# Kernel tuning notes

Measured on AMD Instinct MI355X. Metric: run time of the kernel, lower is better.

## Reference

```python
import jax, jax.numpy as jnp
import numpy as np

B = 512      # number of groups (samples)
SEG = 128    # points per group (fixed for the reference)
N = B * SEG  # total points
E = 64       # embed_size
D = 5 * E    # point feature dim = 320
L = 3        # pointNet blocks
MF = 2       # multiple_factor -> hidden = D*MF = 640
NEG_SLOPE = 0.01


def _leaky(x):
    return jnp.where(x >= 0, x, NEG_SLOPE * x)


def _mlp(x, W1, b1, W2, b2):
    # Linear -> LeakyReLU -> (Dropout=identity, eval) -> Linear -> LeakyReLU
    return _leaky(_leaky(x @ W1 + b1) @ W2 + b2)


def setup_inputs() -> dict:
    key = jax.random.key(0)
    ks = jax.random.split(key, 16)
    s = 0.02
    words = jax.random.randint(ks[0], (N, 5), 0, 26, dtype=jnp.int32)
    lengths = jnp.full((B,), SEG, dtype=jnp.int32)
    seg2all = jnp.repeat(jnp.arange(B, dtype=jnp.int32), SEG)
    inp = {
        "words": words,
        "lengths": lengths,
        "seg2all": seg2all,
        "embed": s * jax.random.normal(ks[1], (26, E), jnp.float32),
        "pu_W1": s * jax.random.normal(ks[2], (L, D, D * MF), jnp.float32),
        "pu_b1": jnp.zeros((L, D * MF), jnp.float32),
        "pu_W2": s * jax.random.normal(ks[3], (L, D * MF, D), jnp.float32),
        "pu_b2": jnp.zeros((L, D), jnp.float32),
        "gu_W1": s * jax.random.normal(ks[4], (L, D, D * MF), jnp.float32),
        "gu_b1": jnp.zeros((L, D * MF), jnp.float32),
        "gu_W2": s * jax.random.normal(ks[5], (L, D * MF, D), jnp.float32),
        "gu_b2": jnp.zeros((L, D), jnp.float32),
        "c_W": s * jax.random.normal(ks[6], (L, 2 * D, D), jnp.float32),
        "c_b": jnp.zeros((L, D), jnp.float32),
        "o_W1": s * jax.random.normal(ks[7], (D, D * MF), jnp.float32),
        "o_b1": jnp.zeros((D * MF,), jnp.float32),
        "o_W2": s * jax.random.normal(ks[8], (D * MF, 1), jnp.float32),
        "o_b2": jnp.zeros((1,), jnp.float32),
        "w": jnp.float32(0.13663686),
    }
    return inp


def reference(words, lengths, seg2all, embed, pu_W1, pu_b1, pu_W2, pu_b2,
              gu_W1, gu_b1, gu_W2, gu_b2, c_W, c_b, o_W1, o_b1, o_W2, o_b2, w):
    inv_len = 1.0 / lengths.astype(jnp.float32)  # [B]

    def seg_mean(x):  # segment_csr(x, offsets, reduce='mean')
        sums = jax.ops.segment_sum(x, seg2all, num_segments=B)
        return sums * inv_len[:, None]

    out = embed[words].reshape(-1, D)  # [N, D]
    for i in range(L):
        h = _mlp(out, pu_W1[i], pu_b1[i], pu_W2[i], pu_b2[i])          # point update
        g = _mlp(seg_mean(h), gu_W1[i], gu_b1[i], gu_W2[i], gu_b2[i])  # group update
        cat = jnp.concatenate([h, g[seg2all]], axis=1)                 # gather-back concat
        out = _leaky(cat @ c_W[i] + c_b[i]) + out                      # combine + residual
    y = _mlp(seg_mean(out), o_W1, o_b1, o_W2, o_b2)  # [B, 1]
    return y.squeeze(-1) + w * jnp.log2(lengths.astype(jnp.float32))
```

## Files before the change

### kernel.cpp

```cpp
#include <hip/hip_runtime.h>
#include <hip/hip_bf16.h>

using bf16 = __hip_bfloat16;
typedef short bf16x8 __attribute__((ext_vector_type(8)));
typedef float f32x4  __attribute__((ext_vector_type(4)));
typedef unsigned short u16;

__device__ __forceinline__ float leakyf(float x) { return x >= 0.f ? x : 0.01f * x; }

__device__ __forceinline__ float b2f(u16 u) {
  union { unsigned int i; float f; } c; c.i = (unsigned int)u << 16; return c.f;
}
__device__ __forceinline__ u16 f2b(float f) {
  __hip_bfloat16 h = __float2bfloat16(f);
  return *reinterpret_cast<u16*>(&h);
}

typedef const __attribute__((address_space(1))) unsigned int* gp_t;
typedef __attribute__((address_space(3))) unsigned int* lp_t;
__device__ __forceinline__ void gload16(const void* g, void* l) {
  __builtin_amdgcn_global_load_lds((gp_t)g, (lp_t)l, 16, 0, 0);
}

__global__ void pack_tiles(const float* __restrict__ pu1, const float* __restrict__ pu2,
                           const float* __restrict__ cw,
                           bf16* __restrict__ W0, bf16* __restrict__ W1t,
                           bf16* __restrict__ W4) {
  int job = blockIdx.y, type = job / 3, l = job % 3;
  int f = blockIdx.x * 256 + threadIdx.x;
  const float* s; bf16* d; int ld, nchunks;
  if (type == 0)      { nchunks = 25600; s = pu1 + (size_t)l * 204800; d = W0  + (size_t)l * 204800; ld = 640; }
  else if (type == 1) { nchunks = 25600; s = pu2 + (size_t)l * 204800; d = W1t + (size_t)l * 204800; ld = 320; }
  else                { nchunks = 12800; s = cw  + (size_t)l * 204800; d = W4  + (size_t)l * 102400; ld = 320; }
  if (f >= nchunks) return;
  int i  = f & 15;
  int ch = (f >> 4) & 7;
  int nt = (f >> 7) % 20;
  int sl = (f >> 7) / 20;
  int k, col;
  if (type == 0) { k = (sl % 5) * 64 + ch * 8; col = (sl / 5) * 320 + nt * 16 + i; }
  else           { k = sl * 64 + ch * 8;       col = nt * 16 + i; }
  bf16 v[8];
#pragma unroll
  for (int j = 0; j < 8; ++j)
    v[j] = __float2bfloat16(s[(size_t)(k + j) * ld + col]);
  *(bf16x8*)(d + (size_t)f * 8) = *(bf16x8*)v;
}

__global__ void pack_nmaj(const float* __restrict__ gu1, const float* __restrict__ gu2,
                          const float* __restrict__ cw, const float* __restrict__ ow1,
                          bf16* __restrict__ Wg1, bf16* __restrict__ Wg2,
                          bf16* __restrict__ Wg3, bf16* __restrict__ Wo1) {
  int job = blockIdx.y;
  int f = blockIdx.x * 256 + threadIdx.x;
  const float* s; bf16* d; int K, ld, nchunks, koff = 0;
  if (job < 3)       { int l = job;     K = 320; ld = 640; nchunks = 25600; s = gu1 + (size_t)l * 204800; d = Wg1 + (size_t)l * 204800; }
  else if (job < 6)  { int l = job - 3; K = 640; ld = 320; nchunks = 25600; s = gu2 + (size_t)l * 204800; d = Wg2 + (size_t)l * 204800; }
  else if (job < 9)  { int l = job - 6; K = 320; ld = 320; nchunks = 12800; s = cw  + (size_t)l * 204800; d = Wg3 + (size_t)l * 102400; koff = 320; }
  else               {                  K = 320; ld = 640; nchunks = 25600; s = ow1;                      d = Wo1; }
  if (f >= nchunks) return;
  int kc8 = K >> 3;
  int n = f / kc8, kc = f % kc8;
  bf16 v[8];
#pragma unroll
  for (int j = 0; j < 8; ++j)
    v[j] = __float2bfloat16(s[(size_t)(koff + kc * 8 + j) * ld + n]);
  *(bf16x8*)(d + (size_t)f * 8) = *(bf16x8*)v;
}

#define PWROW(vv, comp) { int row = rb + vv; \
  *(short*)((char*)p + row * 128 + (col2 ^ ((row & 7) << 4))) = (short)(fq.comp); }

__device__ __forceinline__ void paneWrite4(short* p, ushort4 f0, ushort4 f1,
                                           ushort4 f2, ushort4 f3,
                                           int r, int wc, int i16, int kg) {
  const int col2 = (wc * 16 + i16) * 2;
  { ushort4 fq = f0; int rb = r * 64 + 0  + kg * 4; PWROW(0, x) PWROW(1, y) PWROW(2, z) PWROW(3, w) }
  { ushort4 fq = f1; int rb = r * 64 + 16 + kg * 4; PWROW(0, x) PWROW(1, y) PWROW(2, z) PWROW(3, w) }
  { ushort4 fq = f2; int rb = r * 64 + 32 + kg * 4; PWROW(0, x) PWROW(1, y) PWROW(2, z) PWROW(3, w) }
  { ushort4 fq = f3; int rb = r * 64 + 48 + kg * 4; PWROW(0, x) PWROW(1, y) PWROW(2, z) PWROW(3, w) }
}

__device__ __forceinline__ void stageW(const bf16* src, short* dst, int wave, int lane) {
#pragma unroll
  for (int t = 0; t < 5; ++t) {
    int ci = (t * 8 + wave) * 64 + lane;
    gload16(src + (size_t)ci * 8, (char*)dst + (t * 8 + wave) * 1024);
  }
}

__device__ __forceinline__ void sliceMFMA(f32x4 (&acc)[4][5], const short* pn,
                                          const short* wb,
                                          int r, int wc, int i16, int kg) {
#pragma unroll
  for (int kk = 0; kk < 2; ++kk) {
    bf16x8 a[4];
#pragma unroll
    for (int m = 0; m < 4; ++m) {
      int row = r * 64 + m * 16 + i16;
      a[m] = *(const bf16x8*)((const char*)pn + row * 128 +
                              (((kk * 32 + kg * 8) * 2) ^ ((row & 7) << 4)));
    }
#pragma unroll
    for (int t = 0; t < 5; ++t) {
      bf16x8 b = *(const bf16x8*)((const char*)wb +
                                  (((wc + 4 * t) * 8 + kk * 4 + kg) << 8) + (i16 << 4));
#pragma unroll
      for (int m = 0; m < 4; ++m)
        acc[m][t] = __builtin_amdgcn_mfma_f32_16x16x32_bf16(a[m], b, acc[m][t], 0, 0, 0);
    }
  }
}

__device__ __forceinline__ float dotWrow(const bf16* __restrict__ w,
                                         const float* __restrict__ x, int K8) {
  float s = 0.f;
#pragma unroll 4
  for (int kb = 0; kb < K8; ++kb) {
    bf16x8 wv = *(const bf16x8*)(w + kb * 8);
#pragma unroll
    for (int u = 0; u < 8; ++u)
      s += b2f((u16)wv[u]) * x[kb * 8 + u];
  }
  return s;
}

__device__ __forceinline__ ushort4 pack4(float a, float b, float c, float d) {
  ushort4 u; u.x = f2b(a); u.y = f2b(b); u.z = f2b(c); u.w = f2b(d); return u;
}

__global__ __launch_bounds__(512, 2)
void fused_k(const int* __restrict__ words, const int* __restrict__ lengths,
             const float* __restrict__ embed,
             const bf16* __restrict__ W0, const bf16* __restrict__ W1t,
             const bf16* __restrict__ W4,
             const bf16* __restrict__ Wg1, const bf16* __restrict__ Wg2,
             const bf16* __restrict__ Wg3, const bf16* __restrict__ Wo1,
             const float* __restrict__ pb1, const float* __restrict__ pb2,
             const float* __restrict__ gb1, const float* __restrict__ gb2,
             const float* __restrict__ cb,  const float* __restrict__ ob1,
             const float* __restrict__ oW2, const float* __restrict__ ob2,
             const float* __restrict__ wsc, float* __restrict__ yout)
{
  __shared__ short pane[2][8192];
  __shared__ short wbuf[2][20480];
  __shared__ float embL[1664];
  __shared__ int   wrdL[640];
  __shared__ float mvec[320];
  __shared__ float tvec[640];
  __shared__ float gvec[320];
  __shared__ float redA[320];
  __shared__ float redB[320];
  __shared__ float redH[8];

  const int g    = blockIdx.x;
  const int tid  = threadIdx.x;
  const int wave = tid >> 6, lane = tid & 63;
  const int r    = wave >> 2, wc = wave & 3;
  const int i16  = lane & 15, kg = lane >> 4;
  const float invLen = 1.0f / (float)lengths[g];

  for (int i = tid; i < 1664; i += 512) embL[i] = embed[i];
  { const int* ws = words + (size_t)g * 640;
    for (int i = tid; i < 640; i += 512) wrdL[i] = ws[i]; }
  __syncthreads();

  ushort4 outf[4][5];
#pragma unroll
  for (int m = 0; m < 4; ++m) {
    int row = r * 64 + m * 16 + kg * 4;
#pragma unroll
    for (int t = 0; t < 5; ++t) {
      int col = (wc + 4 * t) * 16 + i16;
      int w = col >> 6, e = col & 63;
      outf[m][t] = pack4(embL[wrdL[(row + 0) * 5 + w] * 64 + e],
                         embL[wrdL[(row + 1) * 5 + w] * 64 + e],
                         embL[wrdL[(row + 2) * 5 + w] * 64 + e],
                         embL[wrdL[(row + 3) * 5 + w] * 64 + e]);
    }
  }

  for (int l = 0; l < 3; ++l) {
    ushort4 h1f[2][4][5];
#pragma unroll
    for (int p = 0; p < 2; ++p) {
      f32x4 acc[4][5];
#pragma unroll
      for (int m = 0; m < 4; ++m)
#pragma unroll
        for (int t = 0; t < 5; ++t) acc[m][t] = {0.f, 0.f, 0.f, 0.f};
      const bf16* wsrc = W0 + ((size_t)(l * 2 + p) * 5) * 20480;
      __syncthreads();
      stageW(wsrc, wbuf[0], wave, lane);
      paneWrite4(pane[0], outf[0][0], outf[1][0], outf[2][0], outf[3][0], r, wc, i16, kg);
#pragma unroll
      for (int ks = 0; ks < 5; ++ks) {
        __syncthreads();
        if (ks < 4) {
          stageW(wsrc + (size_t)(ks + 1) * 20480, wbuf[(ks + 1) & 1], wave, lane);
          paneWrite4(pane[(ks + 1) & 1], outf[0][ks + 1], outf[1][ks + 1],
                     outf[2][ks + 1], outf[3][ks + 1], r, wc, i16, kg);
        }
        sliceMFMA(acc, pane[ks & 1], wbuf[ks & 1], r, wc, i16, kg);
      }
#pragma unroll
      for (int t = 0; t < 5; ++t) {
        int col = p * 320 + (wc + 4 * t) * 16 + i16;
        float bv = pb1[l * 640 + col];
#pragma unroll
        for (int m = 0; m < 4; ++m)
          h1f[p][m][t] = pack4(leakyf(acc[m][t][0] + bv), leakyf(acc[m][t][1] + bv),
                               leakyf(acc[m][t][2] + bv), leakyf(acc[m][t][3] + bv));
      }
    }

    ushort4 hf[4][5];
    {
      f32x4 acc[4][5];
#pragma unroll
      for (int m = 0; m < 4; ++m)
#pragma unroll
        for (int t = 0; t < 5; ++t) acc[m][t] = {0.f, 0.f, 0.f, 0.f};
      const bf16* wsrc = W1t + (size_t)l * 10 * 20480;
      __syncthreads();
      stageW(wsrc, wbuf[0], wave, lane);
      paneWrite4(pane[0], h1f[0][0][0], h1f[0][1][0], h1f[0][2][0], h1f[0][3][0], r, wc, i16, kg);
#pragma unroll
      for (int ks = 0; ks < 10; ++ks) {
        __syncthreads();
        if (ks < 9) {
          stageW(wsrc + (size_t)(ks + 1) * 20480, wbuf[(ks + 1) & 1], wave, lane);
          const int p2 = (ks + 1) / 5, t2 = (ks + 1) % 5;
          paneWrite4(pane[(ks + 1) & 1], h1f[p2][0][t2], h1f[p2][1][t2],
                     h1f[p2][2][t2], h1f[p2][3][t2], r, wc, i16, kg);
        }
        sliceMFMA(acc, pane[ks & 1], wbuf[ks & 1], r, wc, i16, kg);
      }
      __syncthreads();
      float csum[5];
#pragma unroll
      for (int t = 0; t < 5; ++t) {
        int col = (wc + 4 * t) * 16 + i16;
        float bv = pb2[l * 320 + col];
        float v0 = leakyf(acc[0][t][0] + bv), v1 = leakyf(acc[0][t][1] + bv);
        float v2 = leakyf(acc[0][t][2] + bv), v3 = leakyf(acc[0][t][3] + bv);
        float cs = v0 + v1 + v2 + v3;
        hf[0][t] = pack4(v0, v1, v2, v3);
#pragma unroll
        for (int m = 1; m < 4; ++m) {
          float w0 = leakyf(acc[m][t][0] + bv), w1 = leakyf(acc[m][t][1] + bv);
          float w2 = leakyf(acc[m][t][2] + bv), w3 = leakyf(acc[m][t][3] + bv);
          cs += w0 + w1 + w2 + w3;
          hf[m][t] = pack4(w0, w1, w2, w3);
        }
        csum[t] = cs;
      }
#pragma unroll
      for (int t = 0; t < 5; ++t) {
        float s = csum[t];
        s += __shfl_xor(s, 16);
        s += __shfl_xor(s, 32);
        if (kg == 0) (r ? redB : redA)[(wc + 4 * t) * 16 + i16] = s;
      }
      __syncthreads();
      if (tid < 320) mvec[tid] = (redA[tid] + redB[tid]) * invLen;
      __syncthreads();
    }

    tvec[tid] = leakyf(dotWrow(Wg1 + ((size_t)l * 640 + tid) * 320, mvec, 40) +
                       gb1[l * 640 + tid]);
    if (tid < 128) {
      int j2 = 512 + tid;
      tvec[j2] = leakyf(dotWrow(Wg1 + ((size_t)l * 640 + j2) * 320, mvec, 40) +
                        gb1[l * 640 + j2]);
    }
    __syncthreads();
    if (tid < 320)
      gvec[tid] = leakyf(dotWrow(Wg2 + ((size_t)l * 320 + tid) * 640, tvec, 80) +
                         gb2[l * 320 + tid]);
    __syncthreads();
    if (tid < 320)
      tvec[tid] = dotWrow(Wg3 + ((size_t)l * 320 + tid) * 320, gvec, 40) +
                  cb[l * 320 + tid];
    __syncthreads();

    {
      f32x4 acc[4][5];
#pragma unroll
      for (int m = 0; m < 4; ++m)
#pragma unroll
        for (int t = 0; t < 5; ++t) acc[m][t] = {0.f, 0.f, 0.f, 0.f};
      const bf16* wsrc = W4 + (size_t)l * 5 * 20480;
      __syncthreads();
      stageW(wsrc, wbuf[0], wave, lane);
      paneWrite4(pane[0], hf[0][0], hf[1][0], hf[2][0], hf[3][0], r, wc, i16, kg);
#pragma unroll
      for (int ks = 0; ks < 5; ++ks) {
        __syncthreads();
        if (ks < 4) {
          stageW(wsrc + (size_t)(ks + 1) * 20480, wbuf[(ks + 1) & 1], wave, lane);
          paneWrite4(pane[(ks + 1) & 1], hf[0][ks + 1], hf[1][ks + 1],
                     hf[2][ks + 1], hf[3][ks + 1], r, wc, i16, kg);
        }
        sliceMFMA(acc, pane[ks & 1], wbuf[ks & 1], r, wc, i16, kg);
      }
      __syncthreads();
      float csum[5];
#pragma unroll
      for (int t = 0; t < 5; ++t) {
        int col = (wc + 4 * t) * 16 + i16;
        float ga = tvec[col];
        ushort4 ov = outf[0][t];
        float v0 = leakyf(acc[0][t][0] + ga) + b2f(ov.x);
        float v1 = leakyf(acc[0][t][1] + ga) + b2f(ov.y);
        float v2 = leakyf(acc[0][t][2] + ga) + b2f(ov.z);
        float v3 = leakyf(acc[0][t][3] + ga) + b2f(ov.w);
        outf[0][t] = pack4(v0, v1, v2, v3);
        float cs = v0 + v1 + v2 + v3;
#pragma unroll
        for (int m = 1; m < 4; ++m) {
          ushort4 om = outf[m][t];
          float w0 = leakyf(acc[m][t][0] + ga) + b2f(om.x);
          float w1 = leakyf(acc[m][t][1] + ga) + b2f(om.y);
          float w2 = leakyf(acc[m][t][2] + ga) + b2f(om.z);
          float w3 = leakyf(acc[m][t][3] + ga) + b2f(om.w);
          outf[m][t] = pack4(w0, w1, w2, w3);
          cs += w0 + w1 + w2 + w3;
        }
        csum[t] = cs;
      }
#pragma unroll
      for (int t = 0; t < 5; ++t) {
        float s = csum[t];
        s += __shfl_xor(s, 16);
        s += __shfl_xor(s, 32);
        if (kg == 0) (r ? redB : redA)[(wc + 4 * t) * 16 + i16] = s;
      }
      __syncthreads();
      if (tid < 320) mvec[tid] = (redA[tid] + redB[tid]) * invLen;
      __syncthreads();
    }
  }

  tvec[tid] = leakyf(dotWrow(Wo1 + (size_t)tid * 320, mvec, 40) + ob1[tid]);
  if (tid < 128) {
    int j2 = 512 + tid;
    tvec[j2] = leakyf(dotWrow(Wo1 + (size_t)j2 * 320, mvec, 40) + ob1[j2]);
  }
  __syncthreads();
  float part = tvec[tid] * oW2[tid] + (tid < 128 ? tvec[512 + tid] * oW2[512 + tid] : 0.f);
#pragma unroll
  for (int off = 32; off > 0; off >>= 1) part += __shfl_down(part, off);
  if (lane == 0) redH[wave] = part;
  __syncthreads();
  if (tid == 0) {
    float s = 0.f;
#pragma unroll
    for (int w = 0; w < 8; ++w) s += redH[w];
    float y = leakyf(s + ob2[0]);
    yout[g] = y + wsc[0] * log2f((float)lengths[g]);
  }
}

extern "C" void kernel_launch(void* const* d_in, const int* in_sizes, int n_in,
                              void* d_out, int out_size, void* d_ws, size_t ws_size,
                              hipStream_t stream) {
  const int*   words   = (const int*)  d_in[0];
  const int*   lengths = (const int*)  d_in[1];
  const float* embedw  = (const float*)d_in[3];
  const float* pu_W1   = (const float*)d_in[4];
  const float* pu_b1   = (const float*)d_in[5];
  const float* pu_W2   = (const float*)d_in[6];
  const float* pu_b2   = (const float*)d_in[7];
  const float* gu_W1   = (const float*)d_in[8];
  const float* gu_b1   = (const float*)d_in[9];
  const float* gu_W2   = (const float*)d_in[10];
  const float* gu_b2   = (const float*)d_in[11];
  const float* c_W     = (const float*)d_in[12];
  const float* c_b     = (const float*)d_in[13];
  const float* o_W1    = (const float*)d_in[14];
  const float* o_b1    = (const float*)d_in[15];
  const float* o_W2    = (const float*)d_in[16];
  const float* o_b2    = (const float*)d_in[17];
  const float* wscal   = (const float*)d_in[18];

  const int B = in_sizes[1];

  size_t off = 0;
  auto alloc = [&](size_t bytes) -> void* {
    void* p = (char*)d_ws + off;
    off += (bytes + 255) & ~(size_t)255;
    return p;
  };
  bf16* W0  = (bf16*)alloc(614400 * 2);
  bf16* W1t = (bf16*)alloc(614400 * 2);
  bf16* W4  = (bf16*)alloc(307200 * 2);
  bf16* Wg1 = (bf16*)alloc(614400 * 2);
  bf16* Wg2 = (bf16*)alloc(614400 * 2);
  bf16* Wg3 = (bf16*)alloc(307200 * 2);
  bf16* Wo1 = (bf16*)alloc(204800 * 2);

  pack_tiles<<<dim3(100, 9), 256, 0, stream>>>(pu_W1, pu_W2, c_W, W0, W1t, W4);
  pack_nmaj<<<dim3(100, 10), 256, 0, stream>>>(gu_W1, gu_W2, c_W, o_W1,
                                               Wg1, Wg2, Wg3, Wo1);
  fused_k<<<B, 512, 0, stream>>>(words, lengths, embedw, W0, W1t, W4,
                                 Wg1, Wg2, Wg3, Wo1,
                                 pu_b1, pu_b2, gu_b1, gu_b2, c_b, o_b1,
                                 o_W2, o_b2, wscal, (float*)d_out);
}
```

Baseline: 705.2 us.

## Keep activations in LDS, stream weight fragments from global, fuse hidden chunk GEMMs

Activations now stay in a swizzled 128x320 LDS buffer instead of register arrays, and MFMA B fragments are read straight from global/L2 rather than staged through LDS double buffers. The two point-MLP GEMMs are chunked so each 128-column slice of the hidden layer is computed, written to a pane and immediately consumed by the second GEMM. The group-MLP matvecs are split across thread pairs for more parallelism, and launch bounds drop to one block per SM. This removes LDS weight staging and several barriers, but it relies on L2 bandwidth for the weights and lowers occupancy.

```diff
diff --git a/kernel.cpp b/kernel.cpp
--- a/kernel.cpp
+++ b/kernel.cpp
@@ -15,11 +15,42 @@
   __hip_bfloat16 h = __float2bfloat16(f);
   return *reinterpret_cast<u16*>(&h);
 }
-
-typedef const __attribute__((address_space(1))) unsigned int* gp_t;
-typedef __attribute__((address_space(3))) unsigned int* lp_t;
-__device__ __forceinline__ void gload16(const void* g, void* l) {
-  __builtin_amdgcn_global_load_lds((gp_t)g, (lp_t)l, 16, 0, 0);
+__device__ __forceinline__ ushort4 pack4(float a, float b, float c, float d) {
+  ushort4 u; u.x = f2b(a); u.y = f2b(b); u.z = f2b(c); u.w = f2b(d); return u;
+}
+
+__device__ __forceinline__ bf16x8 gfrag(const bf16* __restrict__ p, int gran) {
+  return *(const bf16x8*)(p + ((size_t)gran << 3));
+}
+__device__ __forceinline__ bf16x8 ldsRow(const short* buf, int row, int strideB, int off) {
+  return *(const bf16x8*)((const char*)buf + row * strideB + (off ^ ((row & 7) << 4)));
+}
+__device__ __forceinline__ void scat4(char* base, int row0, int strideB, int col2, ushort4 q) {
+  *(u16*)(base + (row0 + 0) * strideB + (col2 ^ (((row0 + 0) & 7) << 4))) = q.x;
+  *(u16*)(base + (row0 + 1) * strideB + (col2 ^ (((row0 + 1) & 7) << 4))) = q.y;
+  *(u16*)(base + (row0 + 2) * strideB + (col2 ^ (((row0 + 2) & 7) << 4))) = q.z;
+  *(u16*)(base + (row0 + 3) * strideB + (col2 ^ (((row0 + 3) & 7) << 4))) = q.w;
+}
+__device__ __forceinline__ ushort4 gath4(const char* base, int row0, int strideB, int col2) {
+  ushort4 q;
+  q.x = *(const u16*)(base + (row0 + 0) * strideB + (col2 ^ (((row0 + 0) & 7) << 4)));
+  q.y = *(const u16*)(base + (row0 + 1) * strideB + (col2 ^ (((row0 + 1) & 7) << 4)));
+  q.z = *(const u16*)(base + (row0 + 2) * strideB + (col2 ^ (((row0 + 2) & 7) << 4)));
+  q.w = *(const u16*)(base + (row0 + 3) * strideB + (col2 ^ (((row0 + 3) & 7) << 4)));
+  return q;
+}
+
+__device__ __forceinline__ float dotWrow(const bf16* __restrict__ w,
+                                         const float* __restrict__ x, int K8) {
+  float s = 0.f;
+#pragma unroll 4
+  for (int kb = 0; kb < K8; ++kb) {
+    bf16x8 wv = *(const bf16x8*)(w + kb * 8);
+#pragma unroll
+    for (int u = 0; u < 8; ++u)
+      s += b2f((u16)wv[u]) * x[kb * 8 + u];
+  }
+  return s;
 }
 
 __global__ void pack_tiles(const float* __restrict__ pu1, const float* __restrict__ pu2,
@@ -28,23 +59,18 @@
                            bf16* __restrict__ W4) {
   int job = blockIdx.y, type = job / 3, l = job % 3;
   int f = blockIdx.x * 256 + threadIdx.x;
-  const float* s; bf16* d; int ld, nchunks;
-  if (type == 0)      { nchunks = 25600; s = pu1 + (size_t)l * 204800; d = W0  + (size_t)l * 204800; ld = 640; }
-  else if (type == 1) { nchunks = 25600; s = pu2 + (size_t)l * 204800; d = W1t + (size_t)l * 204800; ld = 320; }
-  else                { nchunks = 12800; s = cw  + (size_t)l * 204800; d = W4  + (size_t)l * 102400; ld = 320; }
-  if (f >= nchunks) return;
-  int i  = f & 15;
-  int ch = (f >> 4) & 7;
-  int nt = (f >> 7) % 20;
-  int sl = (f >> 7) / 20;
-  int k, col;
-  if (type == 0) { k = (sl % 5) * 64 + ch * 8; col = (sl / 5) * 320 + nt * 16 + i; }
-  else           { k = sl * 64 + ch * 8;       col = nt * 16 + i; }
-  bf16 v[8];
+  const float* s; bf16* d; int ld, nch, ntn;
+  if (type == 0)      { nch = 25600; s = pu1 + (size_t)l * 204800; d = W0  + (size_t)l * 204800; ld = 640; ntn = 40; }
+  else if (type == 1) { nch = 25600; s = pu2 + (size_t)l * 204800; d = W1t + (size_t)l * 204800; ld = 320; ntn = 20; }
+  else                { nch = 12800; s = cw  + (size_t)l * 204800; d = W4  + (size_t)l * 102400; ld = 320; ntn = 20; }
+  if (f >= nch) return;
+  int i = f & 15, ch = (f >> 4) & 7, nt = (f >> 7) % ntn, ks = (f >> 7) / ntn;
+  int k = ks * 64 + ch * 8, col = nt * 16 + i;
+  bf16x8 v;
 #pragma unroll
   for (int j = 0; j < 8; ++j)
-    v[j] = __float2bfloat16(s[(size_t)(k + j) * ld + col]);
-  *(bf16x8*)(d + (size_t)f * 8) = *(bf16x8*)v;
+    v[j] = (short)f2b(s[(size_t)(k + j) * ld + col]);
+  *(bf16x8*)(d + (size_t)f * 8) = v;
 }
 
 __global__ void pack_nmaj(const float* __restrict__ gu1, const float* __restrict__ gu2,
@@ -53,83 +79,24 @@
                           bf16* __restrict__ Wg3, bf16* __restrict__ Wo1) {
   int job = blockIdx.y;
   int f = blockIdx.x * 256 + threadIdx.x;
-  const float* s; bf16* d; int K, ld, nchunks, koff = 0;
-  if (job < 3)       { int l = job;     K = 320; ld = 640; nchunks = 25600; s = gu1 + (size_t)l * 204800; d = Wg1 + (size_t)l * 204800; }
-  else if (job < 6)  { int l = job - 3; K = 640; ld = 320; nchunks = 25600; s = gu2 + (size_t)l * 204800; d = Wg2 + (size_t)l * 204800; }
-  else if (job < 9)  { int l = job - 6; K = 320; ld = 320; nchunks = 12800; s = cw  + (size_t)l * 204800; d = Wg3 + (size_t)l * 102400; koff = 320; }
-  else               {                  K = 320; ld = 640; nchunks = 25600; s = ow1;                      d = Wo1; }
-  if (f >= nchunks) return;
+  const float* s; bf16* d; int K, ld, nch, koff = 0;
+  if (job < 3)      { int l = job;     K = 320; ld = 640; nch = 25600; s = gu1 + (size_t)l * 204800; d = Wg1 + (size_t)l * 204800; }
+  else if (job < 6) { int l = job - 3; K = 640; ld = 320; nch = 25600; s = gu2 + (size_t)l * 204800; d = Wg2 + (size_t)l * 204800; }
+  else if (job < 9) { int l = job - 6; K = 320; ld = 320; nch = 12800; s = cw  + (size_t)l * 204800; d = Wg3 + (size_t)l * 102400; koff = 320; }
+  else              {                  K = 320; ld = 640; nch = 25600; s = ow1;                      d = Wo1; }
+  if (f >= nch) return;
   int kc8 = K >> 3;
   int n = f / kc8, kc = f % kc8;
-  bf16 v[8];
+  bf16x8 v;
 #pragma unroll
   for (int j = 0; j < 8; ++j)
-    v[j] = __float2bfloat16(s[(size_t)(koff + kc * 8 + j) * ld + n]);
-  *(bf16x8*)(d + (size_t)f * 8) = *(bf16x8*)v;
-}
-
-#define PWROW(vv, comp) { int row = rb + vv; \
-  *(short*)((char*)p + row * 128 + (col2 ^ ((row & 7) << 4))) = (short)(fq.comp); }
-
-__device__ __forceinline__ void paneWrite4(short* p, ushort4 f0, ushort4 f1,
-                                           ushort4 f2, ushort4 f3,
-                                           int r, int wc, int i16, int kg) {
-  const int col2 = (wc * 16 + i16) * 2;
-  { ushort4 fq = f0; int rb = r * 64 + 0  + kg * 4; PWROW(0, x) PWROW(1, y) PWROW(2, z) PWROW(3, w) }
-  { ushort4 fq = f1; int rb = r * 64 + 16 + kg * 4; PWROW(0, x) PWROW(1, y) PWROW(2, z) PWROW(3, w) }
-  { ushort4 fq = f2; int rb = r * 64 + 32 + kg * 4; PWROW(0, x) PWROW(1, y) PWROW(2, z) PWROW(3, w) }
-  { ushort4 fq = f3; int rb = r * 64 + 48 + kg * 4; PWROW(0, x) PWROW(1, y) PWROW(2, z) PWROW(3, w) }
-}
-
-__device__ __forceinline__ void stageW(const bf16* src, short* dst, int wave, int lane) {
-#pragma unroll
-  for (int t = 0; t < 5; ++t) {
-    int ci = (t * 8 + wave) * 64 + lane;
-    gload16(src + (size_t)ci * 8, (char*)dst + (t * 8 + wave) * 1024);
-  }
-}
-
-__device__ __forceinline__ void sliceMFMA(f32x4 (&acc)[4][5], const short* pn,
-                                          const short* wb,
-                                          int r, int wc, int i16, int kg) {
-#pragma unroll
-  for (int kk = 0; kk < 2; ++kk) {
-    bf16x8 a[4];
-#pragma unroll
-    for (int m = 0; m < 4; ++m) {
-      int row = r * 64 + m * 16 + i16;
-      a[m] = *(const bf16x8*)((const char*)pn + row * 128 +
-                              (((kk * 32 + kg * 8) * 2) ^ ((row & 7) << 4)));
-    }
-#pragma unroll
-    for (int t = 0; t < 5; ++t) {
-      bf16x8 b = *(const bf16x8*)((const char*)wb +
-                                  (((wc + 4 * t) * 8 + kk * 4 + kg) << 8) + (i16 << 4));
-#pragma unroll
-      for (int m = 0; m < 4; ++m)
-        acc[m][t] = __builtin_amdgcn_mfma_f32_16x16x32_bf16(a[m], b, acc[m][t], 0, 0, 0);
-    }
-  }
-}
-
-__device__ __forceinline__ float dotWrow(const bf16* __restrict__ w,
-                                         const float* __restrict__ x, int K8) {
-  float s = 0.f;
-#pragma unroll 4
-  for (int kb = 0; kb < K8; ++kb) {
-    bf16x8 wv = *(const bf16x8*)(w + kb * 8);
-#pragma unroll
-    for (int u = 0; u < 8; ++u)
-      s += b2f((u16)wv[u]) * x[kb * 8 + u];
-  }
-  return s;
-}
-
-__device__ __forceinline__ ushort4 pack4(float a, float b, float c, float d) {
-  ushort4 u; u.x = f2b(a); u.y = f2b(b); u.z = f2b(c); u.w = f2b(d); return u;
-}
-
-__global__ __launch_bounds__(512, 2)
+    v[j] = (short)f2b(s[(size_t)(koff + kc * 8 + j) * ld + n]);
+  *(bf16x8*)(d + (size_t)f * 8) = v;
+}
+
+#define MFMA_BF16 __builtin_amdgcn_mfma_f32_16x16x32_bf16
+
+__global__ __launch_bounds__(512, 1)
 void fused_k(const int* __restrict__ words, const int* __restrict__ lengths,
              const float* __restrict__ embed,
              const bf16* __restrict__ W0, const bf16* __restrict__ W1t,
@@ -142,15 +109,13 @@
              const float* __restrict__ oW2, const float* __restrict__ ob2,
              const float* __restrict__ wsc, float* __restrict__ yout)
 {
-  __shared__ short pane[2][8192];
-  __shared__ short wbuf[2][20480];
-  __shared__ float embL[1664];
+  __shared__ short Abuf[128 * 320];
+  __shared__ short pane[2][128 * 128];
   __shared__ int   wrdL[640];
   __shared__ float mvec[320];
   __shared__ float tvec[640];
   __shared__ float gvec[320];
-  __shared__ float redA[320];
-  __shared__ float redB[320];
+  __shared__ float pbuf[640];
   __shared__ float redH[8];
 
   const int g    = blockIdx.x;
@@ -158,188 +123,208 @@
   const int wave = tid >> 6, lane = tid & 63;
   const int r    = wave >> 2, wc = wave & 3;
   const int i16  = lane & 15, kg = lane >> 4;
+  const int r64  = r * 64;
   const float invLen = 1.0f / (float)lengths[g];
 
-  for (int i = tid; i < 1664; i += 512) embL[i] = embed[i];
-  { const int* ws = words + (size_t)g * 640;
-    for (int i = tid; i < 640; i += 512) wrdL[i] = ws[i]; }
+  for (int i = tid; i < 640; i += 512) wrdL[i] = words[(size_t)g * 640 + i];
   __syncthreads();
 
-  ushort4 outf[4][5];
-#pragma unroll
-  for (int m = 0; m < 4; ++m) {
-    int row = r * 64 + m * 16 + kg * 4;
+#pragma unroll
+  for (int q = 0; q < 10; ++q) {
+    int f = q * 512 + tid;
+    int row = f / 40, cc = f - row * 40;
+    int col0 = cc * 8;
+    int w = wrdL[row * 5 + (col0 >> 6)];
+    const float* ep = embed + (size_t)w * 64 + (col0 & 63);
+    bf16x8 v;
+#pragma unroll
+    for (int u = 0; u < 8; ++u) v[u] = (short)f2b(ep[u]);
+    *(bf16x8*)((char*)Abuf + row * 640 + ((cc * 16) ^ ((row & 7) << 4))) = v;
+  }
+  __syncthreads();
+
+  for (int l = 0; l < 3; ++l) {
+    const bf16* W0l  = W0  + (size_t)l * 204800;
+    const bf16* W1l  = W1t + (size_t)l * 204800;
+    const bf16* W4l  = W4  + (size_t)l * 102400;
+    const bf16* Wg1l = Wg1 + (size_t)l * 204800;
+    const bf16* Wg2l = Wg2 + (size_t)l * 204800;
+    const bf16* Wg3l = Wg3 + (size_t)l * 102400;
+
+    f32x4 acc2[4][5];
+#pragma unroll
+    for (int m = 0; m < 4; ++m)
+#pragma unroll
+      for (int t = 0; t < 5; ++t) acc2[m][t] = {0.f, 0.f, 0.f, 0.f};
+
+    for (int c = 0; c < 5; ++c) {
+      short* pn = pane[c & 1];
+      f32x4 acc1[4][2];
+#pragma unroll
+      for (int m = 0; m < 4; ++m) { acc1[m][0] = {0.f,0.f,0.f,0.f}; acc1[m][1] = {0.f,0.f,0.f,0.f}; }
+      const int c8wc = c * 8 + wc;
+#pragma unroll
+      for (int ks = 0; ks < 5; ++ks) {
+#pragma unroll
+        for (int kk = 0; kk < 2; ++kk) {
+          const int off = (ks * 64 + kk * 32 + kg * 8) * 2;
+          bf16x8 a[4];
+#pragma unroll
+          for (int m = 0; m < 4; ++m) a[m] = ldsRow(Abuf, r64 + m * 16 + i16, 640, off);
+          bf16x8 b0 = gfrag(W0l, ((ks * 40 + c8wc)     * 8 + kk * 4 + kg) * 16 + i16);
+          bf16x8 b1 = gfrag(W0l, ((ks * 40 + c8wc + 4) * 8 + kk * 4 + kg) * 16 + i16);
+#pragma unroll
+          for (int m = 0; m < 4; ++m) acc1[m][0] = MFMA_BF16(a[m], b0, acc1[m][0], 0, 0, 0);
+#pragma unroll
+          for (int m = 0; m < 4; ++m) acc1[m][1] = MFMA_BF16(a[m], b1, acc1[m][1], 0, 0, 0);
+        }
+      }
+#pragma unroll
+      for (int tt = 0; tt < 2; ++tt) {
+        const int colg  = c * 128 + (wc + 4 * tt) * 16 + i16;
+        const float bv  = pb1[l * 640 + colg];
+        const int pcol2 = ((wc + 4 * tt) * 16 + i16) * 2;
+#pragma unroll
+        for (int m = 0; m < 4; ++m) {
+          ushort4 hq = pack4(leakyf(acc1[m][tt][0] + bv), leakyf(acc1[m][tt][1] + bv),
+                             leakyf(acc1[m][tt][2] + bv), leakyf(acc1[m][tt][3] + bv));
+          scat4((char*)pn, r64 + m * 16 + kg * 4, 256, pcol2, hq);
+        }
+      }
+      __syncthreads();
+#pragma unroll
+      for (int ss = 0; ss < 2; ++ss) {
+        const int ksg = c * 2 + ss;
+#pragma unroll
+        for (int kk = 0; kk < 2; ++kk) {
+          const int off = (ss * 64 + kk * 32 + kg * 8) * 2;
+          bf16x8 a[4];
+#pragma unroll
+          for (int m = 0; m < 4; ++m) a[m] = ldsRow(pn, r64 + m * 16 + i16, 256, off);
+          bf16x8 b[5];
+#pragma unroll
+          for (int t = 0; t < 5; ++t)
+            b[t] = gfrag(W1l, ((ksg * 20 + wc + 4 * t) * 8 + kk * 4 + kg) * 16 + i16);
+#pragma unroll
+          for (int m = 0; m < 4; ++m)
+#pragma unroll
+            for (int t = 0; t < 5; ++t) acc2[m][t] = MFMA_BF16(a[m], b[t], acc2[m][t], 0, 0, 0);
+        }
+      }
+    }
+
+    ushort4 hf[4][5];
 #pragma unroll
     for (int t = 0; t < 5; ++t) {
-      int col = (wc + 4 * t) * 16 + i16;
-      int w = col >> 6, e = col & 63;
-      outf[m][t] = pack4(embL[wrdL[(row + 0) * 5 + w] * 64 + e],
-                         embL[wrdL[(row + 1) * 5 + w] * 64 + e],
-                         embL[wrdL[(row + 2) * 5 + w] * 64 + e],
-                         embL[wrdL[(row + 3) * 5 + w] * 64 + e]);
-    }
-  }
-
-  for (int l = 0; l < 3; ++l) {
-    ushort4 h1f[2][4][5];
-#pragma unroll
-    for (int p = 0; p < 2; ++p) {
-      f32x4 acc[4][5];
+      const int col = (wc + 4 * t) * 16 + i16;
+      const float bv = pb2[l * 320 + col];
+      float cs = 0.f;
+#pragma unroll
+      for (int m = 0; m < 4; ++m) {
+        float v0 = leakyf(acc2[m][t][0] + bv), v1 = leakyf(acc2[m][t][1] + bv);
+        float v2 = leakyf(acc2[m][t][2] + bv), v3 = leakyf(acc2[m][t][3] + bv);
+        hf[m][t] = pack4(v0, v1, v2, v3);
+        cs += v0 + v1 + v2 + v3;
+      }
+      cs += __shfl_xor(cs, 16);
+      cs += __shfl_xor(cs, 32);
+      if (kg == 0) pbuf[r * 320 + col] = cs;
+    }
+    __syncthreads();
+    if (tid < 320) mvec[tid] = (pbuf[tid] + pbuf[320 + tid]) * invLen;
+    ushort4 outf[4][5];
+#pragma unroll
+    for (int t = 0; t < 5; ++t) {
+      const int col2 = ((wc + 4 * t) * 16 + i16) * 2;
 #pragma unroll
       for (int m = 0; m < 4; ++m)
-#pragma unroll
-        for (int t = 0; t < 5; ++t) acc[m][t] = {0.f, 0.f, 0.f, 0.f};
-      const bf16* wsrc = W0 + ((size_t)(l * 2 + p) * 5) * 20480;
-      __syncthreads();
-      stageW(wsrc, wbuf[0], wave, lane);
-      paneWrite4(pane[0], outf[0][0], outf[1][0], outf[2][0], outf[3][0], r, wc, i16, kg);
-#pragma unroll
-      for (int ks = 0; ks < 5; ++ks) {
-        __syncthreads();
-        if (ks < 4) {
-          stageW(wsrc + (size_t)(ks + 1) * 20480, wbuf[(ks + 1) & 1], wave, lane);
-          paneWrite4(pane[(ks + 1) & 1], outf[0][ks + 1], outf[1][ks + 1],
-                     outf[2][ks + 1], outf[3][ks + 1], r, wc, i16, kg);
-        }
-        sliceMFMA(acc, pane[ks & 1], wbuf[ks & 1], r, wc, i16, kg);
-      }
-#pragma unroll
-      for (int t = 0; t < 5; ++t) {
-        int col = p * 320 + (wc + 4 * t) * 16 + i16;
-        float bv = pb1[l * 640 + col];
-#pragma unroll
-        for (int m = 0; m < 4; ++m)
-          h1f[p][m][t] = pack4(leakyf(acc[m][t][0] + bv), leakyf(acc[m][t][1] + bv),
-                               leakyf(acc[m][t][2] + bv), leakyf(acc[m][t][3] + bv));
-      }
-    }
-
-    ushort4 hf[4][5];
-    {
-      f32x4 acc[4][5];
+        outf[m][t] = gath4((const char*)Abuf, r64 + m * 16 + kg * 4, 640, col2);
+    }
+    __syncthreads();
+
+#pragma unroll
+    for (int t = 0; t < 5; ++t) {
+      const int col2 = ((wc + 4 * t) * 16 + i16) * 2;
 #pragma unroll
       for (int m = 0; m < 4; ++m)
-#pragma unroll
-        for (int t = 0; t < 5; ++t) acc[m][t] = {0.f, 0.f, 0.f, 0.f};
-      const bf16* wsrc = W1t + (size_t)l * 10 * 20480;
-      __syncthreads();
-      stageW(wsrc, wbuf[0], wave, lane);
-      paneWrite4(pane[0], h1f[0][0][0], h1f[0][1][0], h1f[0][2][0], h1f[0][3][0], r, wc, i16, kg);
-#pragma unroll
-      for (int ks = 0; ks < 10; ++ks) {
-        __syncthreads();
-        if (ks < 9) {
-          stageW(wsrc + (size_t)(ks + 1) * 20480, wbuf[(ks + 1) & 1], wave, lane);
-          const int p2 = (ks + 1) / 5, t2 = (ks + 1) % 5;
-          paneWrite4(pane[(ks + 1) & 1], h1f[p2][0][t2], h1f[p2][1][t2],
-                     h1f[p2][2][t2], h1f[p2][3][t2], r, wc, i16, kg);
-        }
-        sliceMFMA(acc, pane[ks & 1], wbuf[ks & 1], r, wc, i16, kg);
-      }
-      __syncthreads();
-      float csum[5];
-#pragma unroll
-      for (int t = 0; t < 5; ++t) {
-        int col = (wc + 4 * t) * 16 + i16;
-        float bv = pb2[l * 320 + col];
-        float v0 = leakyf(acc[0][t][0] + bv), v1 = leakyf(acc[0][t][1] + bv);
-        float v2 = leakyf(acc[0][t][2] + bv), v3 = leakyf(acc[0][t][3] + bv);
-        float cs = v0 + v1 + v2 + v3;
-        hf[0][t] = pack4(v0, v1, v2, v3);
-#pragma unroll
-        for (int m = 1; m < 4; ++m) {
-          float w0 = leakyf(acc[m][t][0] + bv), w1 = leakyf(acc[m][t][1] + bv);
-          float w2 = leakyf(acc[m][t][2] + bv), w3 = leakyf(acc[m][t][3] + bv);
-          cs += w0 + w1 + w2 + w3;
-          hf[m][t] = pack4(w0, w1, w2, w3);
-        }
-        csum[t] = cs;
-      }
-#pragma unroll
-      for (int t = 0; t < 5; ++t) {
-        float s = csum[t];
-        s += __shfl_xor(s, 16);
-        s += __shfl_xor(s, 32);
-        if (kg == 0) (r ? redB : redA)[(wc + 4 * t) * 16 + i16] = s;
-      }
-      __syncthreads();
-      if (tid < 320) mvec[tid] = (redA[tid] + redB[tid]) * invLen;
-      __syncthreads();
-    }
-
-    tvec[tid] = leakyf(dotWrow(Wg1 + ((size_t)l * 640 + tid) * 320, mvec, 40) +
-                       gb1[l * 640 + tid]);
+        scat4((char*)Abuf, r64 + m * 16 + kg * 4, 640, col2, hf[m][t]);
+    }
+    tvec[tid] = leakyf(dotWrow(Wg1l + (size_t)tid * 320, mvec, 40) + gb1[l * 640 + tid]);
     if (tid < 128) {
       int j2 = 512 + tid;
-      tvec[j2] = leakyf(dotWrow(Wg1 + ((size_t)l * 640 + j2) * 320, mvec, 40) +
-                        gb1[l * 640 + j2]);
-    }
-    __syncthreads();
-    if (tid < 320)
-      gvec[tid] = leakyf(dotWrow(Wg2 + ((size_t)l * 320 + tid) * 640, tvec, 80) +
-                         gb2[l * 320 + tid]);
-    __syncthreads();
-    if (tid < 320)
-      tvec[tid] = dotWrow(Wg3 + ((size_t)l * 320 + tid) * 320, gvec, 40) +
-                  cb[l * 320 + tid];
-    __syncthreads();
-
+      tvec[j2] = leakyf(dotWrow(Wg1l + (size_t)j2 * 320, mvec, 40) + gb1[l * 640 + j2]);
+    }
+    __syncthreads();
     {
-      f32x4 acc[4][5];
-#pragma unroll
-      for (int m = 0; m < 4; ++m)
-#pragma unroll
-        for (int t = 0; t < 5; ++t) acc[m][t] = {0.f, 0.f, 0.f, 0.f};
-      const bf16* wsrc = W4 + (size_t)l * 5 * 20480;
-      __syncthreads();
-      stageW(wsrc, wbuf[0], wave, lane);
-      paneWrite4(pane[0], hf[0][0], hf[1][0], hf[2][0], hf[3][0], r, wc, i16, kg);
-#pragma unroll
-      for (int ks = 0; ks < 5; ++ks) {
-        __syncthreads();
-        if (ks < 4) {
-          stageW(wsrc + (size_t)(ks + 1) * 20480, wbuf[(ks + 1) & 1], wave, lane);
-          paneWrite4(pane[(ks + 1) & 1], hf[0][ks + 1], hf[1][ks + 1],
-                     hf[2][ks + 1], hf[3][ks + 1], r, wc, i16, kg);
-        }
-        sliceMFMA(acc, pane[ks & 1], wbuf[ks & 1], r, wc, i16, kg);
-      }
-      __syncthreads();
-      float csum[5];
-#pragma unroll
-      for (int t = 0; t < 5; ++t) {
-        int col = (wc + 4 * t) * 16 + i16;
-        float ga = tvec[col];
-        ushort4 ov = outf[0][t];
-        float v0 = leakyf(acc[0][t][0] + ga) + b2f(ov.x);
-        float v1 = leakyf(acc[0][t][1] + ga) + b2f(ov.y);
-        float v2 = leakyf(acc[0][t][2] + ga) + b2f(ov.z);
-        float v3 = leakyf(acc[0][t][3] + ga) + b2f(ov.w);
-        outf[0][t] = pack4(v0, v1, v2, v3);
-        float cs = v0 + v1 + v2 + v3;
-#pragma unroll
-        for (int m = 1; m < 4; ++m) {
-          ushort4 om = outf[m][t];
-          float w0 = leakyf(acc[m][t][0] + ga) + b2f(om.x);
-          float w1 = leakyf(acc[m][t][1] + ga) + b2f(om.y);
-          float w2 = leakyf(acc[m][t][2] + ga) + b2f(om.z);
-          float w3 = leakyf(acc[m][t][3] + ga) + b2f(om.w);
-          outf[m][t] = pack4(w0, w1, w2, w3);
-          cs += w0 + w1 + w2 + w3;
-        }
-        csum[t] = cs;
-      }
-#pragma unroll
-      for (int t = 0; t < 5; ++t) {
-        float s = csum[t];
-        s += __shfl_xor(s, 16);
-        s += __shfl_xor(s, 32);
-        if (kg == 0) (r ? redB : redA)[(wc + 4 * t) * 16 + i16] = s;
-      }
-      __syncthreads();
-      if (tid < 320) mvec[tid] = (redA[tid] + redB[tid]) * invLen;
-      __syncthreads();
-    }
+      int j = tid >> 1, hh = tid & 1;
+      pbuf[tid] = dotWrow(Wg2l + (size_t)j * 640 + hh * 320, tvec + hh * 320, 40);
+      if (tid < 128) {
+        int u2 = 512 + tid, j2 = u2 >> 1, h2 = u2 & 1;
+        pbuf[u2] = dotWrow(Wg2l + (size_t)j2 * 640 + h2 * 320, tvec + h2 * 320, 40);
+      }
+    }
+    __syncthreads();
+    if (tid < 320) gvec[tid] = leakyf(pbuf[2 * tid] + pbuf[2 * tid + 1] + gb2[l * 320 + tid]);
+    __syncthreads();
+    {
+      int j = tid >> 1, hh = tid & 1;
+      pbuf[tid] = dotWrow(Wg3l + (size_t)j * 320 + hh * 160, gvec + hh * 160, 20);
+      if (tid < 128) {
+        int u2 = 512 + tid, j2 = u2 >> 1, h2 = u2 & 1;
+        pbuf[u2] = dotWrow(Wg3l + (size_t)j2 * 320 + h2 * 160, gvec + h2 * 160, 20);
+      }
+    }
+    __syncthreads();
+    if (tid < 320) tvec[tid] = pbuf[2 * tid] + pbuf[2 * tid + 1] + cb[l * 320 + tid];
+    __syncthreads();
+
+    f32x4 acc3[4][5];
+#pragma unroll
+    for (int m = 0; m < 4; ++m)
+#pragma unroll
+      for (int t = 0; t < 5; ++t) acc3[m][t] = {0.f, 0.f, 0.f, 0.f};
+#pragma unroll
+    for (int ks = 0; ks < 5; ++ks) {
+#pragma unroll
+      for (int kk = 0; kk < 2; ++kk) {
+        const int off = (ks * 64 + kk * 32 + kg * 8) * 2;
+        bf16x8 a[4];
+#pragma unroll
+        for (int m = 0; m < 4; ++m) a[m] = ldsRow(Abuf, r64 + m * 16 + i16, 640, off);
+        bf16x8 b[5];
+#pragma unroll
+        for (int t = 0; t < 5; ++t)
+          b[t] = gfrag(W4l, ((ks * 20 + wc + 4 * t) * 8 + kk * 4 + kg) * 16 + i16);
+#pragma unroll
+        for (int m = 0; m < 4; ++m)
+#pragma unroll
+          for (int t = 0; t < 5; ++t) acc3[m][t] = MFMA_BF16(a[m], b[t], acc3[m][t], 0, 0, 0);
+      }
+    }
+    __syncthreads();
+#pragma unroll
+    for (int t = 0; t < 5; ++t) {
+      const int col = (wc + 4 * t) * 16 + i16;
+      const float ga = tvec[col];
+      const int col2 = col * 2;
+      float cs = 0.f;
+#pragma unroll
+      for (int m = 0; m < 4; ++m) {
+        ushort4 ov = outf[m][t];
+        float v0 = leakyf(acc3[m][t][0] + ga) + b2f(ov.x);
+        float v1 = leakyf(acc3[m][t][1] + ga) + b2f(ov.y);
+        float v2 = leakyf(acc3[m][t][2] + ga) + b2f(ov.z);
+        float v3 = leakyf(acc3[m][t][3] + ga) + b2f(ov.w);
+        scat4((char*)Abuf, r64 + m * 16 + kg * 4, 640, col2, pack4(v0, v1, v2, v3));
+        cs += v0 + v1 + v2 + v3;
+      }
+      cs += __shfl_xor(cs, 16);
+      cs += __shfl_xor(cs, 32);
+      if (kg == 0) pbuf[r * 320 + col] = cs;
+    }
+    __syncthreads();
+    if (tid < 320) mvec[tid] = (pbuf[tid] + pbuf[320 + tid]) * invLen;
+    __syncthreads();
   }
 
   tvec[tid] = leakyf(dotWrow(Wo1 + (size_t)tid * 320, mvec, 40) + ob1[tid]);
@@ -348,7 +333,8 @@
     tvec[j2] = leakyf(dotWrow(Wo1 + (size_t)j2 * 320, mvec, 40) + ob1[j2]);
   }
   __syncthreads();
-  float part = tvec[tid] * oW2[tid] + (tid < 128 ? tvec[512 + tid] * oW2[512 + tid] : 0.f);
+  float part = tvec[tid] * oW2[tid];
+  if (tid < 128) part += tvec[512 + tid] * oW2[512 + tid];
 #pragma unroll
   for (int off = 32; off > 0; off >>= 1) part += __shfl_down(part, off);
   if (lane == 0) redH[wave] = part;
@@ -357,8 +343,7 @@
     float s = 0.f;
 #pragma unroll
     for (int w = 0; w < 8; ++w) s += redH[w];
-    float y = leakyf(s + ob2[0]);
-    yout[g] = y + wsc[0] * log2f((float)lengths[g]);
+    yout[g] = leakyf(s + ob2[0]) + wsc[0] * log2f((float)lengths[g]);
   }
 }
 
@@ -392,13 +377,13 @@
     off += (bytes + 255) & ~(size_t)255;
     return p;
   };
-  bf16* W0  = (bf16*)alloc(614400 * 2);
-  bf16* W1t = (bf16*)alloc(614400 * 2);
-  bf16* W4  = (bf16*)alloc(307200 * 2);
-  bf16* Wg1 = (bf16*)alloc(614400 * 2);
-  bf16* Wg2 = (bf16*)alloc(614400 * 2);
-  bf16* Wg3 = (bf16*)alloc(307200 * 2);
-  bf16* Wo1 = (bf16*)alloc(204800 * 2);
+  bf16* W0  = (bf16*)alloc((size_t)614400 * 2);
+  bf16* W1t = (bf16*)alloc((size_t)614400 * 2);
+  bf16* W4  = (bf16*)alloc((size_t)307200 * 2);
+  bf16* Wg1 = (bf16*)alloc((size_t)614400 * 2);
+  bf16* Wg2 = (bf16*)alloc((size_t)614400 * 2);
+  bf16* Wg3 = (bf16*)alloc((size_t)307200 * 2);
+  bf16* Wo1 = (bf16*)alloc((size_t)204800 * 2);
 
   pack_tiles<<<dim3(100, 9), 256, 0, stream>>>(pu_W1, pu_W2, c_W, W0, W1t, W4);
   pack_nmaj<<<dim3(100, 10), 256, 0, stream>>>(gu_W1, gu_W2, c_W, o_W1,
```

After: 1.182 ms. +67.6%, slower.
